# Kernel tuning notes

Measured on AMD Instinct MI355X. Metric: run time of the kernel, lower is better.

Reference implementation:

```python
import jax, jax.numpy as jnp
import numpy as np

B = 4096
D_IN = 4096
N_REC = 4096
TAU = 20.0
THR = 1.0
DT = 1.0
N_REF = 5
DAMP = 0.3
DECAY = float(np.exp(-DT / TAU))


def spike_function(v_scaled):
    # Heaviside step; gradient (used only in fwdbwd module) is the pseudo-derivative.
    return (v_scaled > 0.0).astype(jnp.float32)


def setup_inputs() -> dict:
    key = jax.random.key(0)
    k1, k2, k3, k4, k5, k6 = jax.random.split(key, 6)
    inputs = jax.random.normal(k1, (B, D_IN), jnp.float32)
    v0 = jax.random.normal(k2, (B, N_REC), jnp.float32) * 0.5
    r0 = jax.random.randint(k3, (B, N_REC), 0, N_REF + 1, jnp.int32)
    z0 = (jax.random.uniform(k4, (B, N_REC)) < 0.1).astype(jnp.float32)  # binary spikes
    # GlorotNormal: std = sqrt(2 / (fan_in + fan_out))
    w_in = (jax.random.normal(k5, (D_IN, N_REC), jnp.float32)
            * np.sqrt(2.0 / (D_IN + N_REC)).astype(np.float32))
    w_rec = (jax.random.normal(k6, (N_REC, N_REC), jnp.float32)
             * np.sqrt(2.0 / (N_REC + N_REC)).astype(np.float32))
    return {"inputs": inputs, "v0": v0, "r0": r0, "z0": z0, "w_in": w_in, "w_rec": w_rec}


def reference(inputs, v0, r0, z0, w_in, w_rec):
    # Zero self-connections (diagonal disconnect mask)
    eye = jnp.eye(N_REC, dtype=w_rec.dtype)
    w_rec_nd = w_rec * (1.0 - eye)

    i_in = inputs @ w_in                    # [B, N_REC]
    i_rec = z0 @ w_rec_nd                   # [B, N_REC]
    i_reset = -THR * z0
    input_current = (1.0 - DECAY) * (i_in + i_rec) + i_reset
    new_v = DECAY * v0 + input_current

    v_scaled = (new_v - THR) / THR
    new_z = spike_function(v_scaled)
    new_z = jnp.where(r0 > 0, 0.0, new_z)   # refractory masking
    new_r = jnp.clip(r0 - 1 + (new_z * N_REF).astype(jnp.int32), 0, N_REF)
    return (new_v, new_z, new_r)
```

## Files before the change

kernel.cpp:

```cpp
#include <hip/hip_runtime.h>
#include <cstdint>
#include <cstddef>


typedef __attribute__((ext_vector_type(8))) _Float16 f16x8;
typedef __attribute__((ext_vector_type(4))) float f32x4;

#define DECAY_F 0.9512294245007140f
#define ONEMD_F 0.0487705754992860f

#define BAR() __builtin_amdgcn_s_barrier()
#define WAITV(n) asm volatile("s_waitcnt vmcnt(" #n ")" ::: "memory")

__device__ __forceinline__ void gl2lds16(const void* g, void* s) {
  __builtin_amdgcn_global_load_lds(
      (const __attribute__((address_space(1))) uint32_t*)g,
      (__attribute__((address_space(3))) uint32_t*)s, 16, 0, 0);
}

__global__ __launch_bounds__(256) void prep_w(const float* __restrict__ w_in,
                                              const float* __restrict__ w_rec,
                                              _Float16* __restrict__ wtH,
                                              _Float16* __restrict__ wtL) {
  __shared__ float s[64][65];
  int bid = blockIdx.x;
  int kt = bid >> 6, nt = bid & 63;
  int k0 = kt * 64, n0 = nt * 64;
  int t = threadIdx.x;

  bool rec = (k0 >= 4096);
  const float* W = rec ? w_rec : w_in;
  int kb = rec ? (k0 - 4096) : k0;

  int cr = t >> 4;
  int cc = (t & 15) * 4;
#pragma unroll
  for (int j = 0; j < 4; ++j) {
    int r = cr + j * 16;
    float4 v = *reinterpret_cast<const float4*>(&W[(size_t)(kb + r) * 4096 + n0 + cc]);
    s[r][cc + 0] = v.x; s[r][cc + 1] = v.y; s[r][cc + 2] = v.z; s[r][cc + 3] = v.w;
  }
  __syncthreads();
#pragma unroll
  for (int j = 0; j < 2; ++j) {
    int g = t + 256 * j;
    int n = g >> 3;
    int k8 = (g & 7) * 8;
    f16x8 h, l;
#pragma unroll
    for (int i = 0; i < 8; ++i) {
      float w = s[k8 + i][n];
      int gk = k0 + k8 + i;
      if (rec && (gk - 4096) == (n0 + n)) w = 0.0f;
      w *= 256.0f;
      _Float16 hi = (_Float16)w;
      h[i] = hi;
      l[i] = (_Float16)(w - (float)hi);
    }
    size_t o = (size_t)(n0 + n) * 8192 + (size_t)(k0 + k8);
    *reinterpret_cast<f16x8*>(&wtH[o]) = h;
    *reinterpret_cast<f16x8*>(&wtL[o]) = l;
  }
}

__global__ __launch_bounds__(256) void prep_a(const float* __restrict__ inputs,
                                              const float* __restrict__ z0,
                                              _Float16* __restrict__ aH,
                                              _Float16* __restrict__ aL) {
  int g = blockIdx.x * 256 + threadIdx.x;
  int b = g >> 9;
  int k8 = (g & 511) * 8;

  const float4* pi = reinterpret_cast<const float4*>(&inputs[(size_t)b * 4096 + k8]);
  float4 x = pi[0], y = pi[1];
  float xs[8] = {x.x, x.y, x.z, x.w, y.x, y.y, y.z, y.w};
  f16x8 h, l;
#pragma unroll
  for (int i = 0; i < 8; ++i) {
    _Float16 hi = (_Float16)xs[i];
    h[i] = hi;
    l[i] = (_Float16)(xs[i] - (float)hi);
  }
  *reinterpret_cast<f16x8*>(&aH[(size_t)b * 8192 + k8]) = h;
  *reinterpret_cast<f16x8*>(&aL[(size_t)b * 4096 + k8]) = l;

  const float4* pz = reinterpret_cast<const float4*>(&z0[(size_t)b * 4096 + k8]);
  x = pz[0]; y = pz[1];
  float zs[8] = {x.x, x.y, x.z, x.w, y.x, y.y, y.z, y.w};
  f16x8 hz;
#pragma unroll
  for (int i = 0; i < 8; ++i) hz[i] = (_Float16)zs[i];
  *reinterpret_cast<f16x8*>(&aH[(size_t)b * 8192 + 4096 + k8]) = hz;
}

#define DO_MFMA(AF, BF, MH, NH)                                              \
  __builtin_amdgcn_s_setprio(1);                                             \
  _Pragma("unroll")                                                          \
  for (int j_ = 0; j_ < 4; ++j_)                                             \
    _Pragma("unroll")                                                        \
    for (int i_ = 0; i_ < 2; ++i_)                                           \
      _Pragma("unroll")                                                      \
      for (int kh_ = 0; kh_ < 2; ++kh_)                                      \
        acc[MH][j_][NH][i_] = __builtin_amdgcn_mfma_f32_16x16x32_f16(        \
            AF[j_][kh_], BF[i_][kh_], acc[MH][j_][NH][i_], 0, 0, 0);         \
  __builtin_amdgcn_s_setprio(0);

__global__ __launch_bounds__(512, 2) void lif_gemm(const _Float16* __restrict__ aH,
                                                   const _Float16* __restrict__ aL,
                                                   const _Float16* __restrict__ wtH,
                                                   const _Float16* __restrict__ wtL,
                                                   float* __restrict__ Sout) {
  extern __shared__ __align__(16) char lds[];

  int bid = blockIdx.x;
  int swz = (bid & 7) * 32 + (bid >> 3);
  int bm = swz >> 4, bn = swz & 15;
  int row0 = bm << 8, col0 = bn << 8;

  int t = threadIdx.x;
  int w = t >> 6, lane = t & 63;
  int wm = w >> 2, wn = w & 3;
  int wm16 = wm << 4, wn16 = wn << 4;
  int rl = lane & 15, klane = lane >> 4;
  int lr = lane >> 3;
  int sg = (lane & 7) ^ lr;

  f32x4 acc[2][4][2][2];
#pragma unroll
  for (int a = 0; a < 2; ++a)
#pragma unroll
    for (int b = 0; b < 4; ++b)
#pragma unroll
      for (int c = 0; c < 2; ++c)
#pragma unroll
        for (int d = 0; d < 2; ++d) acc[a][b][c][d] = (f32x4){0.f, 0.f, 0.f, 0.f};

  auto stageA = [&](int buf, int half, const _Float16* A, int strA, int kb) {
#pragma unroll
    for (int c = 0; c < 2; ++c) {
      int gr = row0 + (half << 7) + (w << 4) + (c << 3) + lr;
      const char* src = (const char*)A + (((size_t)gr * strA + kb) << 1) + (sg << 4);
      char* dst = lds + (buf << 16) + (half << 14) + ((w * 2 + c) << 10);
      gl2lds16(src, dst);
    }
  };
  auto stageB = [&](int buf, int half, const _Float16* Bp, int kb) {
#pragma unroll
    for (int c = 0; c < 2; ++c) {
      int gc = col0 + (half << 7) + (w << 4) + (c << 3) + lr;
      const char* src = (const char*)Bp + (((size_t)gc * 8192 + kb) << 1) + (sg << 4);
      char* dst = lds + (buf << 16) + 32768 + (half << 14) + ((w * 2 + c) << 10);
      gl2lds16(src, dst);
    }
  };
  auto ldsFragA = [&](int buf, int half, int j, int kh) -> f16x8 {
    int r = (j << 5) + wm16 + rl;
    int kb = (kh << 6) + (klane << 4);
    int byte = (buf << 16) + (half << 14) + (r << 7) + (kb ^ ((r & 7) << 4));
    return *(const f16x8*)(lds + byte);
  };
  auto ldsFragB = [&](int buf, int half, int i, int kh) -> f16x8 {
    int r = (i << 6) + wn16 + rl;
    int kb = (kh << 6) + (klane << 4);
    int byte = (buf << 16) + 32768 + (half << 14) + (r << 7) + (kb ^ ((r & 7) << 4));
    return *(const f16x8*)(lds + byte);
  };
  auto segOf = [&](int tt, const _Float16*& A, const _Float16*& Bp, int& kb, int& strA) {
    if (tt < 128)      { A = aH; Bp = wtH; kb = tt << 6;         strA = 8192; }
    else if (tt < 256) { A = aH; Bp = wtL; kb = (tt - 128) << 6; strA = 8192; }
    else               { A = aL; Bp = wtH; kb = (tt - 256) << 6; strA = 4096; }
  };

  {
    const _Float16 *A, *Bp; int kb, strA;
    segOf(0, A, Bp, kb, strA);
    stageA(0, 0, A, strA, kb);
    stageA(0, 1, A, strA, kb);
    stageB(0, 0, Bp, kb);
    stageB(0, 1, Bp, kb);
  }
  WAITV(2);
  BAR();

  f16x8 a0f[4][2], a1f[4][2], b0f[2][2], b1f[2][2];

  for (int tau = 0; tau < 320; ++tau) {
    int cur = tau & 1, nxt = cur ^ 1;
    int nt = tau + 1;
    bool hn = nt < 320;
    const _Float16 *An = aH, *Bn = wtH; int kbn = 0, strAn = 8192;
    if (hn) segOf(nt, An, Bn, kbn, strAn);

#pragma unroll
    for (int j = 0; j < 4; ++j)
#pragma unroll
      for (int kh = 0; kh < 2; ++kh) a0f[j][kh] = ldsFragA(cur, 0, j, kh);
#pragma unroll
    for (int i = 0; i < 2; ++i)
#pragma unroll
      for (int kh = 0; kh < 2; ++kh) b0f[i][kh] = ldsFragB(cur, 0, i, kh);
    if (hn) stageA(nxt, 0, An, strAn, kbn);
    BAR();
    DO_MFMA(a0f, b0f, 0, 0);
    BAR();

#pragma unroll
    for (int j = 0; j < 4; ++j)
#pragma unroll
      for (int kh = 0; kh < 2; ++kh) a1f[j][kh] = ldsFragA(cur, 1, j, kh);
    if (hn) stageA(nxt, 1, An, strAn, kbn);
    BAR();
    DO_MFMA(a1f, b0f, 1, 0);
    if (tau == 319) { WAITV(0); } else { WAITV(4); }
    BAR();

#pragma unroll
    for (int i = 0; i < 2; ++i)
#pragma unroll
      for (int kh = 0; kh < 2; ++kh) b1f[i][kh] = ldsFragB(cur, 1, i, kh);
    if (hn) stageB(nxt, 0, Bn, kbn);
    BAR();
    DO_MFMA(a0f, b1f, 0, 1);
    BAR();

    if (hn) stageB(nxt, 1, Bn, kbn);
    BAR();
    DO_MFMA(a1f, b1f, 1, 1);
    if (hn) { WAITV(2); }
    BAR();
  }

  const float invW = 1.0f / 256.0f;
#pragma unroll
  for (int mh = 0; mh < 2; ++mh)
#pragma unroll
    for (int j = 0; j < 4; ++j)
#pragma unroll
      for (int nh = 0; nh < 2; ++nh)
#pragma unroll
        for (int i = 0; i < 2; ++i) {
          int row = row0 + (mh << 7) + (j << 5) + wm16 + (klane << 2);
          int col = col0 + (nh << 7) + (i << 6) + wn16 + rl;
#pragma unroll
          for (int jj = 0; jj < 4; ++jj)
            Sout[(size_t)(row + jj) * 4096 + col] = acc[mh][j][nh][i][jj] * invW;
        }
}

__global__ __launch_bounds__(256) void lif_epilogue(const float* __restrict__ v0,
                                                    const int* __restrict__ r0,
                                                    const float* __restrict__ z0,
                                                    float* __restrict__ outv,
                                                    float* __restrict__ outz,
                                                    float* __restrict__ outr) {
  size_t i = ((size_t)blockIdx.x * 256 + threadIdx.x) * 4;
  float4 S = *reinterpret_cast<const float4*>(&outv[i]);
  float4 V = *reinterpret_cast<const float4*>(&v0[i]);
  float4 Z = *reinterpret_cast<const float4*>(&z0[i]);
  int4 R = *reinterpret_cast<const int4*>(&r0[i]);
  float s[4] = {S.x, S.y, S.z, S.w};
  float v[4] = {V.x, V.y, V.z, V.w};
  float z[4] = {Z.x, Z.y, Z.z, Z.w};
  int r[4] = {R.x, R.y, R.z, R.w};
  float4 ov, oz, orr;
  float* po[3] = {&ov.x, &oz.x, &orr.x};
#pragma unroll
  for (int j = 0; j < 4; ++j) {
    float nv = DECAY_F * v[j] + (ONEMD_F * s[j] - z[j]);
    bool spike = (nv > 1.0f) && (r[j] <= 0);
    int nr = r[j] - 1 + (spike ? 5 : 0);
    nr = nr < 0 ? 0 : (nr > 5 ? 5 : nr);
    po[0][j] = nv;
    po[1][j] = spike ? 1.0f : 0.0f;
    po[2][j] = (float)nr;
  }
  *reinterpret_cast<float4*>(&outv[i]) = ov;
  *reinterpret_cast<float4*>(&outz[i]) = oz;
  *reinterpret_cast<float4*>(&outr[i]) = orr;
}

extern "C" void kernel_launch(void* const* d_in, const int* in_sizes, int n_in,
                              void* d_out, int out_size, void* d_ws, size_t ws_size,
                              hipStream_t stream) {
  const float* inputs = (const float*)d_in[0];
  const float* v0     = (const float*)d_in[1];
  const int*   r0     = (const int*)d_in[2];
  const float* z0     = (const float*)d_in[3];
  const float* w_in   = (const float*)d_in[4];
  const float* w_rec  = (const float*)d_in[5];

  const size_t planeW = (size_t)4096 * 8192;
  if (ws_size < planeW * 2 * sizeof(_Float16)) return;

  _Float16* wtH = (_Float16*)d_ws;
  _Float16* wtL = wtH + planeW;

  float* out  = (float*)d_out;
  float* outv = out;
  float* outz = out + (size_t)4096 * 4096;
  float* outr = out + (size_t)2 * 4096 * 4096;

  _Float16* aH = (_Float16*)outz;
  _Float16* aL = (_Float16*)outr;

  (void)hipFuncSetAttribute((const void*)lif_gemm,
                            hipFuncAttributeMaxDynamicSharedMemorySize, 131072);

  prep_w<<<dim3(8192), dim3(256), 0, stream>>>(w_in, w_rec, wtH, wtL);
  prep_a<<<dim3(8192), dim3(256), 0, stream>>>(inputs, z0, aH, aL);
  lif_gemm<<<dim3(256), dim3(512), 131072, stream>>>(aH, aL, wtH, wtL, outv);
  lif_epilogue<<<dim3(16384), dim3(256), 0, stream>>>(v0, r0, z0, outv, outz, outr);
}
```

Before: 727.5 us.

## Switch GEMM to 32x32x16 MFMA and fuse LIF epilogue when workspace allows

Replaces the 16x16x32 MFMA tiling with 32x32x16 instructions, which changes the fragment layout, the LDS read pattern and the order of staging and waits in the double-buffered loop. When the workspace is large enough, the A operands move into workspace and the LIF update is fused into the GEMM store, so the separate epilogue kernel and its extra pass over memory go away. The fused store is done per element with strided column-major-ish accesses and non-vectorized loads of v0/r0/z0, and the pipeline's waitcnt changes risk stalls or races.

```diff
diff --git a/kernel.cpp b/kernel.cpp
--- a/kernel.cpp
+++ b/kernel.cpp
@@ -5,6 +5,7 @@
 
 typedef __attribute__((ext_vector_type(8))) _Float16 f16x8;
 typedef __attribute__((ext_vector_type(4))) float f32x4;
+typedef __attribute__((ext_vector_type(16))) float f32x16;
 
 #define DECAY_F 0.9512294245007140f
 #define ONEMD_F 0.0487705754992860f
@@ -96,20 +97,24 @@
 #define DO_MFMA(AF, BF, MH, NH)                                              \
   __builtin_amdgcn_s_setprio(1);                                             \
   _Pragma("unroll")                                                          \
-  for (int j_ = 0; j_ < 4; ++j_)                                             \
+  for (int kc_ = 0; kc_ < 4; ++kc_)                                          \
     _Pragma("unroll")                                                        \
-    for (int i_ = 0; i_ < 2; ++i_)                                           \
-      _Pragma("unroll")                                                      \
-      for (int kh_ = 0; kh_ < 2; ++kh_)                                      \
-        acc[MH][j_][NH][i_] = __builtin_amdgcn_mfma_f32_16x16x32_f16(        \
-            AF[j_][kh_], BF[i_][kh_], acc[MH][j_][NH][i_], 0, 0, 0);         \
+    for (int q_ = 0; q_ < 2; ++q_)                                           \
+      acc[MH][q_][NH] = __builtin_amdgcn_mfma_f32_32x32x16_f16(              \
+          AF[q_][kc_], BF[kc_], acc[MH][q_][NH], 0, 0, 0);                   \
   __builtin_amdgcn_s_setprio(0);
 
+template <int FUSED>
 __global__ __launch_bounds__(512, 2) void lif_gemm(const _Float16* __restrict__ aH,
                                                    const _Float16* __restrict__ aL,
                                                    const _Float16* __restrict__ wtH,
                                                    const _Float16* __restrict__ wtL,
-                                                   float* __restrict__ Sout) {
+                                                   const float* __restrict__ v0,
+                                                   const int* __restrict__ r0,
+                                                   const float* __restrict__ z0,
+                                                   float* __restrict__ o0,
+                                                   float* __restrict__ o1,
+                                                   float* __restrict__ o2) {
   extern __shared__ __align__(16) char lds[];
 
   int bid = blockIdx.x;
@@ -120,20 +125,19 @@
   int t = threadIdx.x;
   int w = t >> 6, lane = t & 63;
   int wm = w >> 2, wn = w & 3;
-  int wm16 = wm << 4, wn16 = wn << 4;
-  int rl = lane & 15, klane = lane >> 4;
+  int l31 = lane & 31, lhi = lane >> 5;
   int lr = lane >> 3;
   int sg = (lane & 7) ^ lr;
 
-  f32x4 acc[2][4][2][2];
+  f32x16 acc[2][2][2];
 #pragma unroll
   for (int a = 0; a < 2; ++a)
 #pragma unroll
-    for (int b = 0; b < 4; ++b)
+    for (int b = 0; b < 2; ++b)
 #pragma unroll
       for (int c = 0; c < 2; ++c)
 #pragma unroll
-        for (int d = 0; d < 2; ++d) acc[a][b][c][d] = (f32x4){0.f, 0.f, 0.f, 0.f};
+        for (int d = 0; d < 16; ++d) acc[a][b][c][d] = 0.0f;
 
   auto stageA = [&](int buf, int half, const _Float16* A, int strA, int kb) {
 #pragma unroll
@@ -153,16 +157,16 @@
       gl2lds16(src, dst);
     }
   };
-  auto ldsFragA = [&](int buf, int half, int j, int kh) -> f16x8 {
-    int r = (j << 5) + wm16 + rl;
-    int kb = (kh << 6) + (klane << 4);
-    int byte = (buf << 16) + (half << 14) + (r << 7) + (kb ^ ((r & 7) << 4));
+  auto ldA = [&](int buf, int mh, int q, int kc) -> f16x8 {
+    int r = (q << 6) + (wm << 5) + l31;
+    int off = (kc << 5) + (lhi << 4);
+    int byte = (buf << 16) + (mh << 14) + (r << 7) + (off ^ ((r & 7) << 4));
     return *(const f16x8*)(lds + byte);
   };
-  auto ldsFragB = [&](int buf, int half, int i, int kh) -> f16x8 {
-    int r = (i << 6) + wn16 + rl;
-    int kb = (kh << 6) + (klane << 4);
-    int byte = (buf << 16) + 32768 + (half << 14) + (r << 7) + (kb ^ ((r & 7) << 4));
+  auto ldB = [&](int buf, int nh, int kc) -> f16x8 {
+    int r = (wn << 5) + l31;
+    int off = (kc << 5) + (lhi << 4);
+    int byte = (buf << 16) + 32768 + (nh << 14) + (r << 7) + (off ^ ((r & 7) << 4));
     return *(const f16x8*)(lds + byte);
   };
   auto segOf = [&](int tt, const _Float16*& A, const _Float16*& Bp, int& kb, int& strA) {
@@ -175,14 +179,14 @@
     const _Float16 *A, *Bp; int kb, strA;
     segOf(0, A, Bp, kb, strA);
     stageA(0, 0, A, strA, kb);
-    stageA(0, 1, A, strA, kb);
     stageB(0, 0, Bp, kb);
     stageB(0, 1, Bp, kb);
-  }
-  WAITV(2);
+    stageA(0, 1, A, strA, kb);
+  }
+  WAITV(4);
   BAR();
 
-  f16x8 a0f[4][2], a1f[4][2], b0f[2][2], b1f[2][2];
+  f16x8 af[2][4], bf0[4], bf1[4];
 
   for (int tau = 0; tau < 320; ++tau) {
     int cur = tau & 1, nxt = cur ^ 1;
@@ -192,41 +196,38 @@
     if (hn) segOf(nt, An, Bn, kbn, strAn);
 
 #pragma unroll
-    for (int j = 0; j < 4; ++j)
-#pragma unroll
-      for (int kh = 0; kh < 2; ++kh) a0f[j][kh] = ldsFragA(cur, 0, j, kh);
-#pragma unroll
-    for (int i = 0; i < 2; ++i)
-#pragma unroll
-      for (int kh = 0; kh < 2; ++kh) b0f[i][kh] = ldsFragB(cur, 0, i, kh);
+    for (int q = 0; q < 2; ++q)
+#pragma unroll
+      for (int kc = 0; kc < 4; ++kc) af[q][kc] = ldA(cur, 0, q, kc);
+#pragma unroll
+    for (int kc = 0; kc < 4; ++kc) bf0[kc] = ldB(cur, 0, kc);
     if (hn) stageA(nxt, 0, An, strAn, kbn);
     BAR();
-    DO_MFMA(a0f, b0f, 0, 0);
-    BAR();
-
-#pragma unroll
-    for (int j = 0; j < 4; ++j)
-#pragma unroll
-      for (int kh = 0; kh < 2; ++kh) a1f[j][kh] = ldsFragA(cur, 1, j, kh);
+    DO_MFMA(af, bf0, 0, 0);
+    WAITV(4);
+    BAR();
+
+#pragma unroll
+    for (int kc = 0; kc < 4; ++kc) bf1[kc] = ldB(cur, 1, kc);
+    if (hn) stageB(nxt, 0, Bn, kbn);
+    BAR();
+    DO_MFMA(af, bf1, 0, 1);
+    WAITV(4);
+    BAR();
+
+#pragma unroll
+    for (int q = 0; q < 2; ++q)
+#pragma unroll
+      for (int kc = 0; kc < 4; ++kc) af[q][kc] = ldA(cur, 1, q, kc);
+    if (hn) stageB(nxt, 1, Bn, kbn);
+    BAR();
+    DO_MFMA(af, bf0, 1, 0);
+    BAR();
+
     if (hn) stageA(nxt, 1, An, strAn, kbn);
     BAR();
-    DO_MFMA(a1f, b0f, 1, 0);
-    if (tau == 319) { WAITV(0); } else { WAITV(4); }
-    BAR();
-
-#pragma unroll
-    for (int i = 0; i < 2; ++i)
-#pragma unroll
-      for (int kh = 0; kh < 2; ++kh) b1f[i][kh] = ldsFragB(cur, 1, i, kh);
-    if (hn) stageB(nxt, 0, Bn, kbn);
-    BAR();
-    DO_MFMA(a0f, b1f, 0, 1);
-    BAR();
-
-    if (hn) stageB(nxt, 1, Bn, kbn);
-    BAR();
-    DO_MFMA(a1f, b1f, 1, 1);
-    if (hn) { WAITV(2); }
+    DO_MFMA(af, bf1, 1, 1);
+    WAITV(4);
     BAR();
   }
 
@@ -234,17 +235,29 @@
 #pragma unroll
   for (int mh = 0; mh < 2; ++mh)
 #pragma unroll
-    for (int j = 0; j < 4; ++j)
-#pragma unroll
-      for (int nh = 0; nh < 2; ++nh)
-#pragma unroll
-        for (int i = 0; i < 2; ++i) {
-          int row = row0 + (mh << 7) + (j << 5) + wm16 + (klane << 2);
-          int col = col0 + (nh << 7) + (i << 6) + wn16 + rl;
-#pragma unroll
-          for (int jj = 0; jj < 4; ++jj)
-            Sout[(size_t)(row + jj) * 4096 + col] = acc[mh][j][nh][i][jj] * invW;
+    for (int q = 0; q < 2; ++q)
+#pragma unroll
+      for (int nh = 0; nh < 2; ++nh) {
+        int gr0 = row0 + (mh << 7) + (q << 6) + (wm << 5) + (lhi << 2);
+        int gc = col0 + (nh << 7) + (wn << 5) + l31;
+#pragma unroll
+        for (int rg = 0; rg < 16; ++rg) {
+          int grow = gr0 + (rg & 3) + ((rg >> 2) << 3);
+          size_t idx = (size_t)grow * 4096 + gc;
+          float S = acc[mh][q][nh][rg] * invW;
+          if (FUSED) {
+            float nv = DECAY_F * v0[idx] + (ONEMD_F * S - z0[idx]);
+            bool spike = (nv > 1.0f) && (r0[idx] <= 0);
+            int nr = r0[idx] - 1 + (spike ? 5 : 0);
+            nr = nr < 0 ? 0 : (nr > 5 ? 5 : nr);
+            o0[idx] = nv;
+            o1[idx] = spike ? 1.0f : 0.0f;
+            o2[idx] = (float)nr;
+          } else {
+            o0[idx] = S;
+          }
         }
+      }
 }
 
 __global__ __launch_bounds__(256) void lif_epilogue(const float* __restrict__ v0,
@@ -289,25 +302,41 @@
   const float* w_in   = (const float*)d_in[4];
   const float* w_rec  = (const float*)d_in[5];
 
-  const size_t planeW = (size_t)4096 * 8192;
-  if (ws_size < planeW * 2 * sizeof(_Float16)) return;
+  const size_t MB = (size_t)1 << 20;
+  if (ws_size < 128 * MB) return;
+  bool fused = (ws_size >= 224 * MB);
 
   _Float16* wtH = (_Float16*)d_ws;
-  _Float16* wtL = wtH + planeW;
+  _Float16* wtL = (_Float16*)((char*)d_ws + 64 * MB);
 
   float* out  = (float*)d_out;
   float* outv = out;
   float* outz = out + (size_t)4096 * 4096;
   float* outr = out + (size_t)2 * 4096 * 4096;
 
-  _Float16* aH = (_Float16*)outz;
-  _Float16* aL = (_Float16*)outr;
-
-  (void)hipFuncSetAttribute((const void*)lif_gemm,
+  _Float16* aH;
+  _Float16* aL;
+  if (fused) {
+    aH = (_Float16*)((char*)d_ws + 128 * MB);
+    aL = (_Float16*)((char*)d_ws + 192 * MB);
+  } else {
+    aH = (_Float16*)outz;
+    aL = (_Float16*)outr;
+  }
+
+  (void)hipFuncSetAttribute((const void*)lif_gemm<1>,
+                            hipFuncAttributeMaxDynamicSharedMemorySize, 131072);
+  (void)hipFuncSetAttribute((const void*)lif_gemm<0>,
                             hipFuncAttributeMaxDynamicSharedMemorySize, 131072);
 
   prep_w<<<dim3(8192), dim3(256), 0, stream>>>(w_in, w_rec, wtH, wtL);
   prep_a<<<dim3(8192), dim3(256), 0, stream>>>(inputs, z0, aH, aL);
-  lif_gemm<<<dim3(256), dim3(512), 131072, stream>>>(aH, aL, wtH, wtL, outv);
-  lif_epilogue<<<dim3(16384), dim3(256), 0, stream>>>(v0, r0, z0, outv, outz, outr);
-}
+  if (fused) {
+    lif_gemm<1><<<dim3(256), dim3(512), 131072, stream>>>(
+        aH, aL, wtH, wtL, v0, r0, z0, outv, outz, outr);
+  } else {
+    lif_gemm<0><<<dim3(256), dim3(512), 131072, stream>>>(
+        aH, aL, wtH, wtL, v0, r0, z0, outv, outz, outr);
+    lif_epilogue<<<dim3(16384), dim3(256), 0, stream>>>(v0, r0, z0, outv, outz, outr);
+  }
+}
```

New measurement: 812.4 us. 1.12x slower.
